# Optimization experiments

Measured on AMD Instinct MI355X. Metric: run time of the kernel, lower is better.

Reference implementation:

```python
import jax, jax.numpy as jnp
import numpy as np
from jax import lax

S = 3000      # number of stocks (and number of targets)
F = 6         # raw features
N = 128       # hidden size
L = 40        # lookback length
L_MAX = 10    # max lag
K = 5         # topk leaders


def setup_inputs() -> dict:
    key = jax.random.key(0)
    ks = jax.random.split(key, 16)
    sc = 1.0 / np.sqrt(N)
    u = lambda k, shp, s=sc: jax.random.uniform(k, shp, jnp.float32, -s, s)
    return {
        "X_scaled": jax.random.normal(ks[0], (1, S, L, F), jnp.float32),
        "X_raw": jax.random.normal(ks[1], (1, S, L, F), jnp.float32),
        "target_idx": jax.random.randint(ks[2], (S,), 0, S, jnp.int32),
        "lstm_Wih": u(ks[3], (4 * N, F)),
        "lstm_Whh": u(ks[4], (4 * N, N)),
        "lstm_bih": u(ks[5], (4 * N,)),
        "lstm_bhh": u(ks[6], (4 * N,)),
        "ln_g": jnp.ones((N,), jnp.float32),
        "ln_b": jnp.zeros((N,), jnp.float32),
        "WQ": u(ks[7], (N, N)),
        "WK": u(ks[8], (N, N)),
        "log_temp": jnp.asarray(np.log(N ** 0.25), jnp.float32),
        "lag_bias": jnp.zeros((L_MAX,), jnp.float32),
        "W1": u(ks[9], (64, 2 * F), 1.0 / np.sqrt(2 * F)),
        "b1": jnp.zeros((64,), jnp.float32),
        "W2": u(ks[10], (32, 64), 1.0 / 8.0),
        "b2": jnp.zeros((32,), jnp.float32),
        "W3": u(ks[11], (1, 32), 1.0 / np.sqrt(32)),
        "b3": jnp.zeros((1,), jnp.float32),
    }


def _lstm(x, Wih, Whh, bih, bhh):
    # x: [BS, L, F] -> hidden sequence [BS, L, N]; torch gate order i,f,g,o
    BS = x.shape[0]
    h0 = jnp.zeros((BS, N), x.dtype)
    bias = bih + bhh

    def step(carry, xt):
        h, c = carry
        g = xt @ Wih.T + h @ Whh.T + bias
        i, f, gg, o = jnp.split(g, 4, axis=-1)
        c = jax.nn.sigmoid(f) * c + jax.nn.sigmoid(i) * jnp.tanh(gg)
        h = jax.nn.sigmoid(o) * jnp.tanh(c)
        return (h, c), h

    _, hs = lax.scan(step, (h0, h0), jnp.swapaxes(x, 0, 1))
    return jnp.swapaxes(hs, 0, 1)


def _ln(x, g, b):
    m = x.mean(-1, keepdims=True)
    v = ((x - m) ** 2).mean(-1, keepdims=True)
    return (x - m) / jnp.sqrt(v + 1e-5) * g + b


def _l2norm(x):
    return x / jnp.clip(jnp.linalg.norm(x, axis=-1, keepdims=True), 1e-12)


def reference(X_scaled, X_raw, target_idx, lstm_Wih, lstm_Whh, lstm_bih,
              lstm_bhh, ln_g, ln_b, WQ, WK, log_temp, lag_bias,
              W1, b1, W2, b2, W3, b3):
    # TemporalEncoder: LSTM over B*S sequences + LayerNorm (B=1)
    H = _ln(_lstm(X_scaled.reshape(S, L, F), lstm_Wih, lstm_Whh,
                  lstm_bih, lstm_bhh), ln_g, ln_b)          # [S, L, N]
    X = X_raw[0]                                            # [S, L, F]

    q = _l2norm(H[target_idx, -1] @ WQ.T)                   # [T, N]
    Hk = _l2norm(H[:, L - L_MAX:] @ WK.T)                   # [S, l_max, N]
    temp = jnp.clip(jnp.exp(log_temp), 0.1, N ** 0.5)

    attn = jnp.einsum('tn,sln->tsl', q, Hk) / temp + lag_bias  # [T, S, l_max]
    self_mask = jnp.arange(S)[None, :] == target_idx[:, None]  # [T, S]
    attn = jnp.where(self_mask[:, :, None], -jnp.inf, attn)

    vals, idx = lax.top_k(attn.reshape(-1, S * L_MAX), K)   # [T, K]
    leader = idx // L_MAX
    lag_j = idx % L_MAX
    lag_pos = jnp.clip(L - 1 - (L_MAX - lag_j), 0, L - 1)

    z = X[leader, lag_pos]                                  # [T, K, F]
    w = jax.nn.softmax(vals, axis=1)
    z_agg = (w[..., None] * z).sum(1)                       # [T, F]
    feat = jnp.concatenate([z_agg, z[:, 0]], axis=-1)       # [T, 2F]

    h1 = jax.nn.relu(feat @ W1.T + b1)
    h2 = jax.nn.relu(h1 @ W2.T + b2)
    return (h2 @ W3.T + b3).squeeze(-1)                     # [T]
```

## Files before the change

### kernel.cpp

```cpp
#include <hip/hip_runtime.h>
#include <math.h>

#define S_N 3000
#define NCOLS 30000
#define SCHUNK 8
#define KTILES 938
#define TPC 118
#define PST 17

typedef __bf16 v8bf __attribute__((ext_vector_type(8)));
typedef float v16f __attribute__((ext_vector_type(16)));
typedef float v4f __attribute__((ext_vector_type(4)));

__device__ __forceinline__ float sigm(float x) { return 1.0f / (1.0f + expf(-x)); }

__device__ __forceinline__ bool bet(float av, int ai, float bv, int bi) {
  return (av > bv) || (av == bv && ai < bi);
}

template <int M>
__device__ __forceinline__ void insS(float (&v)[M], int (&ix)[M], float nv, int ni) {
  if (!(nv > v[M - 1])) return;
  bool b[M];
#pragma unroll
  for (int q = 0; q < M; q++) b[q] = nv > v[q];
#pragma unroll
  for (int q = M - 1; q > 0; q--) {
    v[q]  = b[q] ? (b[q - 1] ? v[q - 1] : nv) : v[q];
    ix[q] = b[q] ? (b[q - 1] ? ix[q - 1] : ni) : ix[q];
  }
  if (b[0]) { v[0] = nv; ix[0] = ni; }
}

template <int M>
__device__ __forceinline__ void insF(float (&v)[M], int (&ix)[M], float nv, int ni) {
  if (!bet(nv, ni, v[M - 1], ix[M - 1])) return;
  bool b[M];
#pragma unroll
  for (int q = 0; q < M; q++) b[q] = bet(nv, ni, v[q], ix[q]);
#pragma unroll
  for (int q = M - 1; q > 0; q--) {
    v[q]  = b[q] ? (b[q - 1] ? v[q - 1] : nv) : v[q];
    ix[q] = b[q] ? (b[q - 1] ? ix[q - 1] : ni) : ix[q];
  }
  if (b[0]) { v[0] = nv; ix[0] = ni; }
}

__device__ __forceinline__ unsigned short f2bf_rne(float f) {
  unsigned int u = __float_as_uint(f);
  unsigned int r = (u + 0x7fffu + ((u >> 16) & 1u)) >> 16;
  return (unsigned short)r;
}
__device__ __forceinline__ float bf2f(unsigned short h) {
  return __uint_as_float(((unsigned int)h) << 16);
}

__global__ __launch_bounds__(256) void cvt_wll(
    const float* __restrict__ Whh, unsigned short* __restrict__ Wllf)
{
  int idx = blockIdx.x * 256 + threadIdx.x;
  if (idx >= 128 * 512) return;
  int f = idx >> 9;
  int lane = (idx >> 3) & 63;
  int j = idx & 7;
  int w = f >> 3, tau = (f >> 1) & 3, s = f & 1;
  int kh = w >> 3, g8 = w & 7;
  int gate = g8 * 64 + tau * 16 + (lane & 15);
  int k = kh * 64 + s * 32 + (lane >> 4) * 8 + j;
  float x = Whh[gate * 128 + k];
  unsigned short hi = f2bf_rne(x);
  float r1 = x - bf2f(hi);
  unsigned short lo = f2bf_rne(r1);
  float r2 = r1 - bf2f(lo);
  Wllf[idx] = f2bf_rne(r2);
}

__global__ __launch_bounds__(1024, 4) void lstm_kernel(
    const float* __restrict__ Xs, const float* __restrict__ Wih,
    const float* __restrict__ Whh, const float* __restrict__ bih,
    const float* __restrict__ bhh, const unsigned short* __restrict__ Wllf,
    float* __restrict__ H10)
{
  __shared__ float P[2 * 512 * PST];
  __shared__ __align__(16) __bf16 Asp[3][4][65][8];
  __shared__ __align__(16) float Xb8[12 * 41 * 8];
  __shared__ float2 WB2[14][128];

  const int tid = threadIdx.x;
  const int s0 = blockIdx.x * 12;
  const int lane = tid & 63;
  const int wv = tid >> 6;
  const int kh = wv >> 3;
  const int g8 = wv & 7;
  const int l15 = lane & 15, lq = lane >> 4;

  for (int i = tid; i < 12 * 40 * 8; i += 1024) {
    int m = i / 320, r = i - m * 320, t = r >> 3, f = r & 7;
    Xb8[(m * 41 + t) * 8 + f] =
        (f < 6) ? Xs[(size_t)(s0 + m) * 240 + t * 6 + f] : 0.0f;
  }
  for (int i = tid; i < 3 * 4 * 65 * 8; i += 1024)
    ((unsigned short*)Asp)[i] = 0;
  for (int i = tid; i < 14 * 128; i += 1024) {
    int q = i >> 7, n = i & 127;
    float vv[2];
#pragma unroll
    for (int e = 0; e < 2; e++) {
      int r = 2 * q + e;
      if (r < 24) {
        int gate = n + (r / 6) * 128;
        vv[e] = Wih[gate * 6 + r % 6];
      } else {
        int gate = n + (r - 24) * 128;
        vv[e] = bih[gate] + bhh[gate];
      }
    }
    WB2[q][n] = make_float2(vv[0], vv[1]);
  }

  v8bf whi[4][2], wlo[4][2];
#pragma unroll
  for (int tau = 0; tau < 4; tau++)
#pragma unroll
    for (int s = 0; s < 2; s++) {
      int gate = g8 * 64 + tau * 16 + l15;
      int k0 = kh * 64 + s * 32 + lq * 8;
      const float* wp = Whh + gate * 128 + k0;
      v8bf h8, l8;
#pragma unroll
      for (int j = 0; j < 8; j++) {
        float x = wp[j];
        __bf16 bh_ = (__bf16)x;
        float r1 = x - (float)bh_;
        __bf16 bl_ = (__bf16)r1;
        h8[j] = bh_;
        l8[j] = bl_;
      }
      whi[tau][s] = h8;
      wlo[tau][s] = l8;
    }

  const unsigned short* wllbase = Wllf + (size_t)(wv * 8) * 512 + lane * 8;

  float c0 = 0.0f, c1 = 0.0f;
  const int p2n = tid & 127;
  const int p2m = tid >> 7;
  const int rdrow = (lane & 48) | ((lane + 2 * (lane >> 4)) & 15);

  __syncthreads();

#pragma unroll 1
  for (int t = 0; t < 40; t++) {
    v8bf ah[2], al[2], a3[2];
#pragma unroll
    for (int s = 0; s < 2; s++) {
      int ks = kh * 2 + s;
      ah[s] = *(const v8bf*)&Asp[0][ks][rdrow][0];
      al[s] = *(const v8bf*)&Asp[1][ks][rdrow][0];
      a3[s] = *(const v8bf*)&Asp[2][ks][rdrow][0];
    }
#pragma unroll
    for (int tau = 0; tau < 4; tau++) {
      v4f acc = {0.0f, 0.0f, 0.0f, 0.0f};
#pragma unroll
      for (int s = 0; s < 2; s++) {
        v8bf wll = *(const v8bf*)(wllbase + (tau * 2 + s) * 512);
        acc = __builtin_amdgcn_mfma_f32_16x16x32_bf16(ah[s], whi[tau][s], acc, 0, 0, 0);
        acc = __builtin_amdgcn_mfma_f32_16x16x32_bf16(ah[s], wlo[tau][s], acc, 0, 0, 0);
        acc = __builtin_amdgcn_mfma_f32_16x16x32_bf16(al[s], whi[tau][s], acc, 0, 0, 0);
        acc = __builtin_amdgcn_mfma_f32_16x16x32_bf16(al[s], wlo[tau][s], acc, 0, 0, 0);
        acc = __builtin_amdgcn_mfma_f32_16x16x32_bf16(ah[s], wll, acc, 0, 0, 0);
        acc = __builtin_amdgcn_mfma_f32_16x16x32_bf16(a3[s], whi[tau][s], acc, 0, 0, 0);
      }
      if (lq < 3) {
        int gate = g8 * 64 + tau * 16 + l15;
        float* pp = P + kh * (512 * PST) + gate * PST + lq * 4;
#pragma unroll
        for (int reg = 0; reg < 4; reg++) pp[reg] = acc[reg];
      }
    }
    __syncthreads();

    float wb[28];
#pragma unroll
    for (int q = 0; q < 14; q++) {
      float2 v = WB2[q][p2n];
      wb[2 * q] = v.x;
      wb[2 * q + 1] = v.y;
    }
#pragma unroll
    for (int task = 0; task < 2; task++) {
      if (task == 1 && tid >= 512) break;
      const int m = task == 0 ? p2m : 8 + p2m;
      const int n = p2n;
      float4 xa = *(const float4*)(Xb8 + (m * 41 + t) * 8);
      float4 xbv = *(const float4*)(Xb8 + (m * 41 + t) * 8 + 4);
      float xv[6] = {xa.x, xa.y, xa.z, xa.w, xbv.x, xbv.y};
      float g4[4];
#pragma unroll
      for (int g = 0; g < 4; g++) {
        float a = wb[24 + g];
#pragma unroll
        for (int f = 0; f < 6; f++) a = fmaf(wb[g * 6 + f], xv[f], a);
        int gate = n + g * 128;
        a += P[gate * PST + m] + P[512 * PST + gate * PST + m];
        g4[g] = a;
      }
      float& c = task == 0 ? c0 : c1;
      c = sigm(g4[1]) * c + sigm(g4[0]) * tanhf(g4[2]);
      float h = sigm(g4[3]) * tanhf(c);
      if (t >= 30) H10[((size_t)(s0 + m) * 10 + (t - 30)) * 128 + n] = h;
      __bf16 hh = (__bf16)h;
      float r1 = h - (float)hh;
      __bf16 hl = (__bf16)r1;
      float r2 = r1 - (float)hl;
      __bf16 h3 = (__bf16)r2;
      int g = (n >> 3) & 3;
      int ks = n >> 5;
      int j = n & 7;
      int row = 16 * g + ((m + 2 * g) & 15);
      Asp[0][ks][row][j] = hh;
      Asp[1][ks][row][j] = hl;
      Asp[2][ks][row][j] = h3;
    }
    __syncthreads();
  }
}

__global__ __launch_bounds__(256) void proj_kernel(
    const float* __restrict__ In, const float* __restrict__ WK,
    const float* __restrict__ WQ, const float* __restrict__ lng,
    const float* __restrict__ lnb, float* __restrict__ Kn,
    float* __restrict__ Qn, unsigned short* __restrict__ Qhi,
    unsigned short* __restrict__ Qlo)
{
  __shared__ float A_s[16 * 128];
  const int tid = threadIdx.x;
  const int bk = blockIdx.x;
  const bool isQ = bk >= 1875;
  const int inOff = isQ ? 9 * 128 : 0;
  const int inStride = isQ ? 1280 : 128;
  const int nr = isQ ? 3000 : 30000;
  const float* W = isQ ? WQ : WK;
  float* Out = isQ ? Qn : Kn;
  unsigned short* OutHi = isQ ? Qhi : nullptr;
  unsigned short* OutLo = isQ ? Qlo : nullptr;
  const int r0 = (isQ ? bk - 1875 : bk) * 16;

  for (int i = tid; i < 16 * 32; i += 256) {
    int row = i >> 5, c = i & 31;
    int gr = r0 + row;
    float4 v = make_float4(0.f, 0.f, 0.f, 0.f);
    if (gr < nr)
      v = *(const float4*)(In + (size_t)inOff + (size_t)gr * inStride + c * 4);
    *(float4*)(A_s + row * 128 + c * 4) = v;
  }
  __syncthreads();

  {
    const int wvv = tid >> 6, lane = tid & 63;
    const float g0 = lng[lane], g1 = lng[lane + 64];
    const float bb0 = lnb[lane], bb1 = lnb[lane + 64];
#pragma unroll
    for (int p = 0; p < 4; p++) {
      float* hr = A_s + (wvv * 4 + p) * 128;
      float x0 = hr[lane], x1 = hr[lane + 64];
      float s = x0 + x1;
      for (int off = 32; off > 0; off >>= 1) s += __shfl_xor(s, off);
      float mean = s * (1.0f / 128.0f);
      float d0 = x0 - mean, d1 = x1 - mean;
      float v = d0 * d0 + d1 * d1;
      for (int off = 32; off > 0; off >>= 1) v += __shfl_xor(v, off);
      float rstd = 1.0f / sqrtf(v * (1.0f / 128.0f) + 1e-5f);
      hr[lane] = d0 * rstd * g0 + bb0;
      hr[lane + 64] = d1 * rstd * g1 + bb1;
    }
  }
  __syncthreads();

  const int j = tid & 127, rh = tid >> 7;
  const float* wrow = W + j * 128;
  float acc[8] = {0, 0, 0, 0, 0, 0, 0, 0};
  for (int kc = 0; kc < 32; kc++) {
    float4 wv4 = *(const float4*)(wrow + kc * 4);
#pragma unroll
    for (int i = 0; i < 8; i++) {
      float4 a4 = *(const float4*)(A_s + (rh * 8 + i) * 128 + kc * 4);
      acc[i] = fmaf(wv4.x, a4.x, acc[i]);
      acc[i] = fmaf(wv4.y, a4.y, acc[i]);
      acc[i] = fmaf(wv4.z, a4.z, acc[i]);
      acc[i] = fmaf(wv4.w, a4.w, acc[i]);
    }
  }
  __syncthreads();
#pragma unroll
  for (int i = 0; i < 8; i++) A_s[(rh * 8 + i) * 128 + j] = acc[i];
  __syncthreads();

  const int r = tid >> 4, qq = tid & 15;
  float ss = 0.0f;
#pragma unroll
  for (int i = 0; i < 8; i++) {
    float u = A_s[r * 128 + qq + i * 16];
    ss += u * u;
  }
  for (int off = 8; off > 0; off >>= 1) ss += __shfl_xor(ss, off);
  float scale = 1.0f / fmaxf(sqrtf(ss), 1e-12f);
  int gr = r0 + r;
  if (gr < nr) {
#pragma unroll
    for (int i = 0; i < 8; i++) {
      float val = A_s[r * 128 + qq + i * 16] * scale;
      int col = qq + i * 16;
      Out[(size_t)gr * 128 + col] = val;
      if (OutHi) {
        unsigned short h = f2bf_rne(val);
        unsigned short l = f2bf_rne(val - bf2f(h));
        OutHi[(size_t)gr * 128 + col] = h;
        OutLo[(size_t)gr * 128 + col] = l;
      }
    }
  }
}

__global__ __launch_bounds__(256) void cvt_blockK(
    const float* __restrict__ Kn, unsigned short* __restrict__ hi,
    unsigned short* __restrict__ lo)
{
  const int tile = blockIdx.x;
  const int tid = threadIdx.x;
#pragma unroll
  for (int jj = 0; jj < 4; jj++) {
    int i = tid + jj * 256;
    int r = i >> 5;
    int c0 = (i & 31) * 4;
    int row = tile * 32 + r;
    if (row >= NCOLS) continue;
    float4 f = *(const float4*)(Kn + (size_t)row * 128 + c0);
    ushort4 h, l;
    h.x = f2bf_rne(f.x); l.x = f2bf_rne(f.x - bf2f(h.x));
    h.y = f2bf_rne(f.y); l.y = f2bf_rne(f.y - bf2f(h.y));
    h.z = f2bf_rne(f.z); l.z = f2bf_rne(f.z - bf2f(h.z));
    h.w = f2bf_rne(f.w); l.w = f2bf_rne(f.w - bf2f(h.w));
    int s = c0 >> 4, half = (c0 >> 3) & 1, e = c0 & 7;
    size_t idx = (size_t)tile * 4096 + s * 512 + half * 256 + r * 8 + e;
    *(ushort4*)(hi + idx) = h;
    *(ushort4*)(lo + idx) = l;
  }
}

__global__ __launch_bounds__(256, 3) void score_mfma(
    const unsigned short* __restrict__ Qh, const unsigned short* __restrict__ Ql,
    const unsigned short* __restrict__ Kh, const unsigned short* __restrict__ Kl,
    const int* __restrict__ tix, const float* __restrict__ log_temp,
    const float* __restrict__ lag_bias, float* __restrict__ part)
{
  __shared__ float lagS2[42];
  __shared__ float M[256 * 16];
  const int tid = threadIdx.x;
  const int wv = tid >> 6, lane = tid & 63;
  const int half = lane >> 5, tcol = lane & 31;

  const int lid = blockIdx.y * 94 + blockIdx.x;
  const int chunk = lid & 7;
  const int T0 = (lid >> 3) * 32;
  const int tstart = chunk * TPC;
  const int tend = (tstart + TPC < KTILES) ? tstart + TPC : KTILES;

  for (int i = tid; i < 42; i += 256) lagS2[i] = lag_bias[i % 10];

  const int tgt = T0 + tcol;
  const int tgtc = tgt < S_N ? tgt : S_N - 1;
  const int myTix = tix[tgtc];
  const int selfLo = myTix * 10;
  const float invtemp =
      1.0f / fminf(fmaxf(expf(log_temp[0]), 0.1f), 11.313708499f);

  v8bf bh[8], bl[8];
  {
    const size_t qo = (size_t)myTix * 128 + half * 8;
#pragma unroll
    for (int s = 0; s < 8; s++) {
      bh[s] = *(const v8bf*)(Qh + qo + s * 16);
      bl[s] = *(const v8bf*)(Ql + qo + s * 16);
    }
  }
#pragma unroll
  for (int s = 0; s < 8; s++) {
    asm volatile("" : "+v"(bh[s]), "+v"(bl[s]));
  }

  float tv[8]; int ti[8];
#pragma unroll
  for (int q = 0; q < 8; q++) { tv[q] = -3e38f; ti[q] = 0x7fffffff; }

  __syncthreads();

  for (int it = 0; it < 30; it++) {
    const int tile = tstart + it * 4 + wv;
    const int tilec = tile < KTILES ? tile : KTILES - 1;
    const size_t ao = (size_t)tilec * 4096 + half * 256 + tcol * 8;

    v16f acc0, acc1;
#pragma unroll
    for (int q = 0; q < 16; q++) { acc0[q] = 0.0f; acc1[q] = 0.0f; }

#pragma unroll
    for (int s = 0; s < 8; s++) {
      v8bf ah = *(const v8bf*)(Kh + ao + s * 512);
      v8bf al = *(const v8bf*)(Kl + ao + s * 512);
      acc0 = __builtin_amdgcn_mfma_f32_32x32x16_bf16(ah, bh[s], acc0, 0, 0, 0);
      acc1 = __builtin_amdgcn_mfma_f32_32x32x16_bf16(ah, bl[s], acc1, 0, 0, 0);
      acc1 = __builtin_amdgcn_mfma_f32_32x32x16_bf16(al, bh[s], acc1, 0, 0, 0);
    }

    const int cb = tile * 32;
    const int m0 = cb % 10;
    const bool act = tile < tend;
#pragma unroll
    for (int reg = 0; reg < 16; reg++) {
      const int row = (reg & 3) + 8 * (reg >> 2) + 4 * half;
      const int col = cb + row;
      float vsc = fmaf(acc0[reg] + acc1[reg], invtemp, lagS2[m0 + row]);
      if (act && col < NCOLS && (unsigned)(col - selfLo) >= 10u)
        insS<8>(tv, ti, vsc, col);
    }
  }

  {
    float* my = M + tid * 16;
#pragma unroll
    for (int q = 0; q < 8; q++) {
      my[2 * q] = tv[q];
      my[2 * q + 1] = __int_as_float(ti[q]);
    }
  }
  __syncthreads();
  if (tid < 32 && T0 + tid < S_N) {
    float v[8]; int ix[8];
#pragma unroll
    for (int q = 0; q < 8; q++) { v[q] = -3e38f; ix[q] = 0x7fffffff; }
    for (int w = 0; w < 8; w++) {
      const float* src = M + (w * 32 + tid) * 16;
#pragma unroll
      for (int q = 0; q < 8; q++)
        insF<8>(v, ix, src[2 * q], __float_as_int(src[2 * q + 1]));
    }
    float* dst = part + ((size_t)(T0 + tid) * SCHUNK + chunk) * 16;
#pragma unroll
    for (int q = 0; q < 8; q++) {
      dst[2 * q] = v[q];
      dst[2 * q + 1] = __int_as_float(ix[q]);
    }
  }
}

__global__ __launch_bounds__(256) void final_kernel(
    const float* __restrict__ part, const float* __restrict__ Qn,
    const float* __restrict__ Kn, const int* __restrict__ tix,
    const float* __restrict__ log_temp, const float* __restrict__ lag_bias,
    const float* __restrict__ Xraw,
    const float* __restrict__ W1, const float* __restrict__ b1,
    const float* __restrict__ W2, const float* __restrict__ b2,
    const float* __restrict__ W3, const float* __restrict__ b3,
    float* __restrict__ out)
{
  __shared__ float W1s[64 * 12];
  __shared__ float W2s[32 * 64];
  __shared__ float b1s[64];
  __shared__ float b2s[32];
  __shared__ float W3s[32];
  const int tid = threadIdx.x;
  for (int i = tid; i < 768; i += 256) W1s[i] = W1[i];
  for (int i = tid; i < 2048; i += 256) W2s[i] = W2[i];
  if (tid < 64) b1s[tid] = b1[tid];
  if (tid < 32) { b2s[tid] = b2[tid]; W3s[tid] = W3[tid]; }
  __syncthreads();

  int t = blockIdx.x * 256 + tid;
  if (t >= S_N) return;

  float av[8]; int ai[8];
#pragma unroll
  for (int q = 0; q < 8; q++) { av[q] = -3e38f; ai[q] = 0x7fffffff; }
  const float* pp = part + (size_t)t * (SCHUNK * 16);
  for (int c = 0; c < SCHUNK * 8; c++)
    insF<8>(av, ai, pp[2 * c], __float_as_int(pp[2 * c + 1]));

  const float invtemp =
      1.0f / fminf(fmaxf(expf(log_temp[0]), 0.1f), 11.313708499f);
  const float* q = Qn + (size_t)tix[t] * 128;
  const float* kr[8];
#pragma unroll
  for (int j = 0; j < 8; j++) kr[j] = Kn + (size_t)ai[j] * 128;
  float d[8] = {0, 0, 0, 0, 0, 0, 0, 0};
  for (int kc = 0; kc < 32; kc++) {
    float4 q4 = ((const float4*)q)[kc];
#pragma unroll
    for (int j = 0; j < 8; j++) {
      float4 k4 = ((const float4*)kr[j])[kc];
      d[j] = fmaf(q4.x, k4.x, d[j]);
      d[j] = fmaf(q4.y, k4.y, d[j]);
      d[j] = fmaf(q4.z, k4.z, d[j]);
      d[j] = fmaf(q4.w, k4.w, d[j]);
    }
  }

  float v[5]; int ix[5];
#pragma unroll
  for (int qq = 0; qq < 5; qq++) { v[qq] = -3e38f; ix[qq] = 0x7fffffff; }
#pragma unroll
  for (int j = 0; j < 8; j++) {
    int c = ai[j];
    int s = c / 10;
    int lag = c - 10 * s;
    float ev = d[j] * invtemp + lag_bias[lag];
    insF<5>(v, ix, ev, c);
  }

  float e1 = expf(v[1] - v[0]), e2 = expf(v[2] - v[0]),
        e3 = expf(v[3] - v[0]), e4 = expf(v[4] - v[0]);
  float rs = 1.0f / (1.0f + e1 + e2 + e3 + e4);
  float w_[5] = {rs, e1 * rs, e2 * rs, e3 * rs, e4 * rs};

  float feat[12];
#pragma unroll
  for (int f = 0; f < 12; f++) feat[f] = 0.0f;
#pragma unroll
  for (int qq = 0; qq < 5; qq++) {
    int iq = ix[qq];
    int s = iq / 10;
    int l = iq - 10 * s;
    int pos = 29 + l;
    const float* zp = Xraw + (size_t)s * 240 + pos * 6;
#pragma unroll
    for (int f = 0; f < 6; f++) {
      float z = zp[f];
      feat[f] += w_[qq] * z;
      if (qq == 0) feat[6 + f] = z;
    }
  }

  float h1[64];
#pragma unroll 4
  for (int o = 0; o < 64; o++) {
    float acc = b1s[o];
    const float* wr = W1s + o * 12;
#pragma unroll
    for (int f = 0; f < 12; f++) acc = fmaf(wr[f], feat[f], acc);
    h1[o] = fmaxf(acc, 0.0f);
  }
  float rr = b3[0];
#pragma unroll 2
  for (int o = 0; o < 32; o++) {
    float acc = b2s[o];
    const float* wr = W2s + o * 64;
#pragma unroll 8
    for (int k = 0; k < 64; k++) acc = fmaf(wr[k], h1[k], acc);
    rr = fmaf(W3s[o], fmaxf(acc, 0.0f), rr);
  }
  out[t] = rr;
}

extern "C" void kernel_launch(void* const* d_in, const int* in_sizes, int n_in,
                              void* d_out, int out_size, void* d_ws,
                              size_t ws_size, hipStream_t stream) {
  const float* Xs   = (const float*)d_in[0];
  const float* Xraw = (const float*)d_in[1];
  const int*   tix  = (const int*)d_in[2];
  const float* Wih  = (const float*)d_in[3];
  const float* Whh  = (const float*)d_in[4];
  const float* bih  = (const float*)d_in[5];
  const float* bhh  = (const float*)d_in[6];
  const float* ln_g = (const float*)d_in[7];
  const float* ln_b = (const float*)d_in[8];
  const float* WQ   = (const float*)d_in[9];
  const float* WK   = (const float*)d_in[10];
  const float* log_temp = (const float*)d_in[11];
  const float* lag_bias = (const float*)d_in[12];
  const float* W1 = (const float*)d_in[13];
  const float* b1 = (const float*)d_in[14];
  const float* W2 = (const float*)d_in[15];
  const float* b2 = (const float*)d_in[16];
  const float* W3 = (const float*)d_in[17];
  const float* b3 = (const float*)d_in[18];
  float* outp = (float*)d_out;

  float* ws = (float*)d_ws;
  float* H10 = ws;
  unsigned short* Khi = (unsigned short*)ws;
  unsigned short* Klo = (unsigned short*)(ws + 1922000);
  float* Kn  = ws + 3850000;
  float* Qn  = ws + 7690000;
  unsigned short* Qhi = (unsigned short*)(ws + 8074000);
  unsigned short* Qlo = (unsigned short*)(ws + 8266000);
  float* part = ws + 8458000;
  unsigned short* Wllf = (unsigned short*)(ws + 9226000);

  cvt_wll<<<256, 256, 0, stream>>>(Whh, Wllf);
  lstm_kernel<<<250, 1024, 0, stream>>>(Xs, Wih, Whh, bih, bhh, Wllf, H10);
  proj_kernel<<<2063, 256, 0, stream>>>(H10, WK, WQ, ln_g, ln_b, Kn, Qn,
                                        Qhi, Qlo);
  cvt_blockK<<<KTILES, 256, 0, stream>>>(Kn, Khi, Klo);
  {
    dim3 grid(94, SCHUNK);
    score_mfma<<<grid, 256, 0, stream>>>(Qhi, Qlo, Khi, Klo, tix, log_temp,
                                         lag_bias, part);
  }
  final_kernel<<<12, 256, 0, stream>>>(part, Qn, Kn, tix, log_temp, lag_bias,
                                       Xraw, W1, b1, W2, b2, W3, b3, outp);
}
```

Measured before the change: 670.0 us.

## Process two 32-target groups per score block to reuse key tile loads

Each score_mfma block now handles 64 targets, as two sets of query fragments, against the same streamed key tiles. The grid is halved, so each hi/lo key tile load feeds six MFMAs instead of three, cutting global key traffic. The cost is roughly double the register use for query fragments and top-k state, with launch bounds lowered to 2 blocks per CU, and a larger shared buffer for the merge step. The accumulator split also changes from acc0+acc1 to one combined accumulator per target group.

```diff
diff --git a/kernel.cpp b/kernel.cpp
--- a/kernel.cpp
+++ b/kernel.cpp
@@ -349,50 +349,56 @@
   }
 }
 
-__global__ __launch_bounds__(256, 3) void score_mfma(
+__global__ __launch_bounds__(256, 2) void score_mfma(
     const unsigned short* __restrict__ Qh, const unsigned short* __restrict__ Ql,
     const unsigned short* __restrict__ Kh, const unsigned short* __restrict__ Kl,
     const int* __restrict__ tix, const float* __restrict__ log_temp,
     const float* __restrict__ lag_bias, float* __restrict__ part)
 {
   __shared__ float lagS2[42];
-  __shared__ float M[256 * 16];
+  __shared__ float M[256 * 32];
   const int tid = threadIdx.x;
   const int wv = tid >> 6, lane = tid & 63;
   const int half = lane >> 5, tcol = lane & 31;
 
-  const int lid = blockIdx.y * 94 + blockIdx.x;
+  const int lid = blockIdx.y * 47 + blockIdx.x;
   const int chunk = lid & 7;
-  const int T0 = (lid >> 3) * 32;
+  const int T0 = (lid >> 3) * 64;
   const int tstart = chunk * TPC;
   const int tend = (tstart + TPC < KTILES) ? tstart + TPC : KTILES;
 
   for (int i = tid; i < 42; i += 256) lagS2[i] = lag_bias[i % 10];
 
-  const int tgt = T0 + tcol;
-  const int tgtc = tgt < S_N ? tgt : S_N - 1;
-  const int myTix = tix[tgtc];
-  const int selfLo = myTix * 10;
   const float invtemp =
       1.0f / fminf(fmaxf(expf(log_temp[0]), 0.1f), 11.313708499f);
 
-  v8bf bh[8], bl[8];
-  {
+  int selfLo[2];
+  v8bf bh[2][8], bl[2][8];
+#pragma unroll
+  for (int s2 = 0; s2 < 2; s2++) {
+    int tgt = T0 + s2 * 32 + tcol;
+    int tgtc = tgt < S_N ? tgt : S_N - 1;
+    int myTix = tix[tgtc];
+    selfLo[s2] = myTix * 10;
     const size_t qo = (size_t)myTix * 128 + half * 8;
 #pragma unroll
     for (int s = 0; s < 8; s++) {
-      bh[s] = *(const v8bf*)(Qh + qo + s * 16);
-      bl[s] = *(const v8bf*)(Ql + qo + s * 16);
-    }
-  }
-#pragma unroll
-  for (int s = 0; s < 8; s++) {
-    asm volatile("" : "+v"(bh[s]), "+v"(bl[s]));
-  }
-
-  float tv[8]; int ti[8];
-#pragma unroll
-  for (int q = 0; q < 8; q++) { tv[q] = -3e38f; ti[q] = 0x7fffffff; }
+      bh[s2][s] = *(const v8bf*)(Qh + qo + s * 16);
+      bl[s2][s] = *(const v8bf*)(Ql + qo + s * 16);
+    }
+  }
+#pragma unroll
+  for (int s2 = 0; s2 < 2; s2++)
+#pragma unroll
+    for (int s = 0; s < 8; s++) {
+      asm volatile("" : "+v"(bh[s2][s]), "+v"(bl[s2][s]));
+    }
+
+  float tv[2][8]; int ti[2][8];
+#pragma unroll
+  for (int s2 = 0; s2 < 2; s2++)
+#pragma unroll
+    for (int q = 0; q < 8; q++) { tv[s2][q] = -3e38f; ti[s2][q] = 0x7fffffff; }
 
   __syncthreads();
 
@@ -401,17 +407,20 @@
     const int tilec = tile < KTILES ? tile : KTILES - 1;
     const size_t ao = (size_t)tilec * 4096 + half * 256 + tcol * 8;
 
-    v16f acc0, acc1;
-#pragma unroll
-    for (int q = 0; q < 16; q++) { acc0[q] = 0.0f; acc1[q] = 0.0f; }
+    v16f accA, accB;
+#pragma unroll
+    for (int q = 0; q < 16; q++) { accA[q] = 0.0f; accB[q] = 0.0f; }
 
 #pragma unroll
     for (int s = 0; s < 8; s++) {
       v8bf ah = *(const v8bf*)(Kh + ao + s * 512);
       v8bf al = *(const v8bf*)(Kl + ao + s * 512);
-      acc0 = __builtin_amdgcn_mfma_f32_32x32x16_bf16(ah, bh[s], acc0, 0, 0, 0);
-      acc1 = __builtin_amdgcn_mfma_f32_32x32x16_bf16(ah, bl[s], acc1, 0, 0, 0);
-      acc1 = __builtin_amdgcn_mfma_f32_32x32x16_bf16(al, bh[s], acc1, 0, 0, 0);
+      accA = __builtin_amdgcn_mfma_f32_32x32x16_bf16(ah, bh[0][s], accA, 0, 0, 0);
+      accA = __builtin_amdgcn_mfma_f32_32x32x16_bf16(ah, bl[0][s], accA, 0, 0, 0);
+      accA = __builtin_amdgcn_mfma_f32_32x32x16_bf16(al, bh[0][s], accA, 0, 0, 0);
+      accB = __builtin_amdgcn_mfma_f32_32x32x16_bf16(ah, bh[1][s], accB, 0, 0, 0);
+      accB = __builtin_amdgcn_mfma_f32_32x32x16_bf16(ah, bl[1][s], accB, 0, 0, 0);
+      accB = __builtin_amdgcn_mfma_f32_32x32x16_bf16(al, bh[1][s], accB, 0, 0, 0);
     }
 
     const int cb = tile * 32;
@@ -421,27 +430,34 @@
     for (int reg = 0; reg < 16; reg++) {
       const int row = (reg & 3) + 8 * (reg >> 2) + 4 * half;
       const int col = cb + row;
-      float vsc = fmaf(acc0[reg] + acc1[reg], invtemp, lagS2[m0 + row]);
-      if (act && col < NCOLS && (unsigned)(col - selfLo) >= 10u)
-        insS<8>(tv, ti, vsc, col);
+      const float lag = lagS2[m0 + row];
+      float v0 = fmaf(accA[reg], invtemp, lag);
+      float v1 = fmaf(accB[reg], invtemp, lag);
+      if (act && col < NCOLS) {
+        if ((unsigned)(col - selfLo[0]) >= 10u) insS<8>(tv[0], ti[0], v0, col);
+        if ((unsigned)(col - selfLo[1]) >= 10u) insS<8>(tv[1], ti[1], v1, col);
+      }
     }
   }
 
   {
-    float* my = M + tid * 16;
-#pragma unroll
-    for (int q = 0; q < 8; q++) {
-      my[2 * q] = tv[q];
-      my[2 * q + 1] = __int_as_float(ti[q]);
-    }
-  }
-  __syncthreads();
-  if (tid < 32 && T0 + tid < S_N) {
+    float* my = M + tid * 32;
+#pragma unroll
+    for (int s2 = 0; s2 < 2; s2++)
+#pragma unroll
+      for (int q = 0; q < 8; q++) {
+        my[s2 * 16 + 2 * q] = tv[s2][q];
+        my[s2 * 16 + 2 * q + 1] = __int_as_float(ti[s2][q]);
+      }
+  }
+  __syncthreads();
+  if (tid < 64 && T0 + tid < S_N) {
+    const int s2 = tid >> 5, lc = tid & 31;
     float v[8]; int ix[8];
 #pragma unroll
     for (int q = 0; q < 8; q++) { v[q] = -3e38f; ix[q] = 0x7fffffff; }
     for (int w = 0; w < 8; w++) {
-      const float* src = M + (w * 32 + tid) * 16;
+      const float* src = M + ((w >> 1) * 64 + (w & 1) * 32 + lc) * 32 + s2 * 16;
 #pragma unroll
       for (int q = 0; q < 8; q++)
         insF<8>(v, ix, src[2 * q], __float_as_int(src[2 * q + 1]));
@@ -603,7 +619,7 @@
                                         Qhi, Qlo);
   cvt_blockK<<<KTILES, 256, 0, stream>>>(Kn, Khi, Klo);
   {
-    dim3 grid(94, SCHUNK);
+    dim3 grid(47, SCHUNK);
     score_mfma<<<grid, 256, 0, stream>>>(Qhi, Qlo, Khi, Klo, tix, log_temp,
                                          lag_bias, part);
   }
```

After: 736.4 us. 9.9% more time.
